# Optimization experiments

Hardware: AMD Instinct MI355X
Metric: run time of the kernel (lower is better)

The kernel has to match this reference:

```python
import jax, jax.numpy as jnp
import numpy as np

B, S, E, H = 4, 2048, 1024, 16
D = E // H
FF = 4096
LN_EPS = 1e-3  # Keras LayerNormalization default epsilon


def _layernorm(x, g, b):
    mu = jnp.mean(x, axis=-1, keepdims=True)
    var = jnp.mean(jnp.square(x - mu), axis=-1, keepdims=True)
    return (x - mu) * jax.lax.rsqrt(var + LN_EPS) * g + b


def setup_inputs() -> dict:
    key = jax.random.key(0)
    ks = jax.random.split(key, 16)
    s = lambda fan_in: 1.0 / np.sqrt(fan_in)
    inp = {
        "x": jax.random.normal(ks[0], (B, S, E), jnp.float32),
        "mask": jnp.ones((B, S), dtype=bool),
        "Wq": jax.random.normal(ks[1], (E, E), jnp.float32) * s(E),
        "bq": jnp.zeros((E,), jnp.float32),
        "Wk": jax.random.normal(ks[2], (E, E), jnp.float32) * s(E),
        "bk": jnp.zeros((E,), jnp.float32),
        "Wv": jax.random.normal(ks[3], (E, E), jnp.float32) * s(E),
        "bv": jnp.zeros((E,), jnp.float32),
        "Wo": jax.random.normal(ks[4], (E, E), jnp.float32) * s(E),
        "bo": jnp.zeros((E,), jnp.float32),
        "W1": jax.random.normal(ks[5], (E, FF), jnp.float32) * s(E),
        "b1": jnp.zeros((FF,), jnp.float32),
        "W2": jax.random.normal(ks[6], (FF, E), jnp.float32) * s(FF),
        "b2": jnp.zeros((E,), jnp.float32),
        "ln1_g": jnp.ones((E,), jnp.float32),
        "ln1_b": jnp.zeros((E,), jnp.float32),
        "ln2_g": jnp.ones((E,), jnp.float32),
        "ln2_b": jnp.zeros((E,), jnp.float32),
    }
    return inp


def reference(x, mask, Wq, bq, Wk, bk, Wv, bv, Wo, bo, W1, b1, W2, b2,
              ln1_g, ln1_b, ln2_g, ln2_b):
    # --- multi-head self attention (manual matmul + softmax + matmul) ---
    def heads(t):  # [B,S,E] -> [B,H,S,D]
        return t.reshape(B, S, H, D).transpose(0, 2, 1, 3)

    q = heads(x @ Wq + bq)
    k = heads(x @ Wk + bk)
    v = heads(x @ Wv + bv)

    scores = jnp.einsum("bhqd,bhkd->bhqk", q, k) / jnp.sqrt(jnp.float32(D))
    m = mask.astype(jnp.float32)[:, None, None, :]  # [B,1,1,S]
    scores = scores + (-1e9) * (1.0 - m)
    weights = jax.nn.softmax(scores, axis=-1)
    attn = jnp.einsum("bhqk,bhkd->bhqd", weights, v)
    attn = attn.transpose(0, 2, 1, 3).reshape(B, S, E)
    attn = attn @ Wo + bo

    # residual + layernorm (dropout is identity: training=False)
    h = _layernorm(x + attn, ln1_g, ln1_b)

    # --- FFN ---
    ff = jax.nn.relu(h @ W1 + b1) @ W2 + b2
    out = _layernorm(h + ff, ln2_g, ln2_b)
    return out
```

## Files before the change

### kernel.cpp

```cpp
#include <hip/hip_runtime.h>
#include <stdint.h>
#include <stddef.h>

#define Bn 4
#define Sn 2048
#define En 1024
#define Hn 16
#define Dn 64
#define FFn 4096
#define Mn (Bn*Sn)

typedef __bf16 bf16_t;
typedef __bf16 bf16x8 __attribute__((ext_vector_type(8)));
typedef __bf16 bf16x4 __attribute__((ext_vector_type(4)));
typedef float  f32x4  __attribute__((ext_vector_type(4)));
typedef float  f32x16 __attribute__((ext_vector_type(16)));

#define AS1 __attribute__((address_space(1)))
#define AS3 __attribute__((address_space(3)))

#define EXP2F(x) __builtin_amdgcn_exp2f(x)

static __device__ __forceinline__ void gload_lds16(const bf16_t* g, void* l) {
    __builtin_amdgcn_global_load_lds((const AS1 void*)g, (AS3 void*)l, 16, 0, 0);
}

__global__ __launch_bounds__(256)
void cvt_bf16(const float* __restrict__ xin, bf16_t* __restrict__ xout, int n)
{
    int i = (blockIdx.x * 256 + threadIdx.x) * 4;
    if (i >= n) return;
    float4 f = *(const float4*)(xin + i);
    bf16x4 o;
    o[0] = (bf16_t)f.x; o[1] = (bf16_t)f.y; o[2] = (bf16_t)f.z; o[3] = (bf16_t)f.w;
    *(bf16x4*)(xout + i) = o;
}

__global__ __launch_bounds__(256)
void transp_bf16(const float* __restrict__ W, bf16_t* __restrict__ WT, int R, int C)
{
    __shared__ float t[32][33];
    const int tx = threadIdx.x & 31, ty = threadIdx.x >> 5;
    const int c0 = blockIdx.x * 32, r0 = blockIdx.y * 32;
    #pragma unroll
    for (int i = ty; i < 32; i += 8)
        t[i][tx] = W[(size_t)(r0 + i) * C + c0 + tx];
    __syncthreads();
    #pragma unroll
    for (int i = ty; i < 32; i += 8)
        WT[(size_t)(c0 + i) * R + r0 + tx] = (bf16_t)t[tx][i];
}

__global__ __launch_bounds__(256)
void concat_bias(const float* __restrict__ a, const float* __restrict__ b,
                 const float* __restrict__ c, float* __restrict__ o)
{
    int i = blockIdx.x * 256 + threadIdx.x;
    o[i] = (i < 1024) ? a[i] : ((i < 2048) ? b[i - 1024] : c[i - 2048]);
}

template<int MODE>
__global__ __launch_bounds__(512)
void gemm3r(const bf16_t* __restrict__ A, const bf16_t* __restrict__ BT,
            const float* __restrict__ bias,
            float* __restrict__ Cf, bf16_t* __restrict__ Cb,
            int Ndim, int Kdim)
{
    extern __shared__ char smem[];
    bf16_t* lA = (bf16_t*)smem;
    bf16_t* lB = (bf16_t*)(smem + 3 * 256 * 64 * 2);

    const int tid = threadIdx.x, lane = tid & 63;
    const int w = tid >> 6, wm = w >> 1, wn = w & 1;
    const int bm = blockIdx.y, bn = blockIdx.x;

    const int srow = tid >> 3;
    const int ssl  = tid & 7;
    const int swz  = (ssl ^ (srow & 7)) * 8;
    const bf16_t* Ab = A  + (size_t)(bm * 256 + srow) * Kdim + swz;
    const bf16_t* Bb = BT + (size_t)(bn * 128 + srow) * Kdim + swz;
    const int ldst = srow * 64 + ssl * 8;

    const int ntiles = Kdim >> 6;

    f32x4 acc[4][4] = {};

    const int arow0 = (wm * 64 + (lane & 15)) * 64;
    const int brow0 = (wn * 64 + (lane & 15)) * 64;
    const int g0 = (((lane >> 4)    ) ^ (lane & 7)) * 8;
    const int g1 = ((4 + (lane >> 4)) ^ (lane & 7)) * 8;

    #define STAGE3(r, kt) do {                                                  \
        bf16_t* a_ = lA + (r) * (256 * 64) + ldst;                              \
        bf16_t* b_ = lB + (r) * (128 * 64) + ldst;                              \
        const bf16_t* ga_ = Ab + (kt) * 64;                                     \
        const bf16_t* gb_ = Bb + (kt) * 64;                                     \
        gload_lds16(ga_,                          a_);                          \
        gload_lds16(ga_ + (size_t)64  * Kdim,     a_ + 64 * 64);                \
        gload_lds16(ga_ + (size_t)128 * Kdim,     a_ + 128 * 64);               \
        gload_lds16(ga_ + (size_t)192 * Kdim,     a_ + 192 * 64);               \
        gload_lds16(gb_,                          b_);                          \
        gload_lds16(gb_ + (size_t)64  * Kdim,     b_ + 64 * 64);                \
    } while (0)

    STAGE3(0, 0);
    STAGE3(1, 1);

    for (int t = 0; t < ntiles; ++t) {
        if (t + 2 < ntiles) asm volatile("s_waitcnt vmcnt(6)" ::: "memory");
        else                asm volatile("s_waitcnt vmcnt(0)" ::: "memory");
        __builtin_amdgcn_s_barrier();
        __builtin_amdgcn_sched_barrier(0);
        if (t + 2 < ntiles) STAGE3((t + 2) % 3, t + 2);

        const bf16_t* pa = lA + (t % 3) * (256 * 64) + arow0;
        const bf16_t* pb = lB + (t % 3) * (128 * 64) + brow0;
        bf16x8 aF[4][2], bF[4][2];
        #pragma unroll
        for (int m = 0; m < 4; ++m) {
            aF[m][0] = *(const bf16x8*)(pa + m * 16 * 64 + g0);
            aF[m][1] = *(const bf16x8*)(pa + m * 16 * 64 + g1);
        }
        #pragma unroll
        for (int n = 0; n < 4; ++n) {
            bF[n][0] = *(const bf16x8*)(pb + n * 16 * 64 + g0);
            bF[n][1] = *(const bf16x8*)(pb + n * 16 * 64 + g1);
        }
        __builtin_amdgcn_s_setprio(1);
        #pragma unroll
        for (int m = 0; m < 4; ++m)
            #pragma unroll
            for (int n = 0; n < 4; ++n) {
                acc[m][n] = __builtin_amdgcn_mfma_f32_16x16x32_bf16(
                                aF[m][0], bF[n][0], acc[m][n], 0, 0, 0);
                acc[m][n] = __builtin_amdgcn_mfma_f32_16x16x32_bf16(
                                aF[m][1], bF[n][1], acc[m][n], 0, 0, 0);
            }
        __builtin_amdgcn_s_setprio(0);
    }
    #undef STAGE3

    const size_t ME = (size_t)Mn * En;
    const int fc = lane & 15;
    const int fr = (lane >> 4) * 4;
    #pragma unroll
    for (int n = 0; n < 4; ++n) {
        const int gcol = bn * 128 + wn * 64 + n * 16 + fc;
        const float bv = bias[gcol];
        #pragma unroll
        for (int m = 0; m < 4; ++m) {
            const int growb = bm * 256 + wm * 64 + m * 16 + fr;
            #pragma unroll
            for (int j = 0; j < 4; ++j) {
                const int grow = growb + j;
                float v = acc[m][n][j] + bv;
                if constexpr (MODE == 0) {
                    Cf[(size_t)grow * Ndim + gcol] = v;
                } else if constexpr (MODE == 2) {
                    Cb[(size_t)grow * Ndim + gcol] = (bf16_t)fmaxf(v, 0.f);
                } else {
                    const int id = gcol >> 10;
                    const int c1 = gcol & 1023;
                    const int b = grow >> 11, s = grow & 2047;
                    const int h = c1 >> 6,    d = c1 & 63;
                    if (id < 2)
                        Cb[(size_t)id * ME + (((size_t)(b * 16 + h) << 11) + s) * 64 + d] = (bf16_t)v;
                    else
                        Cb[2 * ME + (((size_t)(b * 16 + h) * 64 + d) << 11) + s] = (bf16_t)v;
                }
            }
        }
    }
}

static __device__ __forceinline__ uint32_t pack2_bf16(float a, float b) {
    union { bf16_t h[2]; uint32_t u; } v;
    v.h[0] = (bf16_t)a; v.h[1] = (bf16_t)b;
    return v.u;
}

#define PSWAP(a,b) asm volatile("v_permlane32_swap_b32 %0, %1" : "+v"(a), "+v"(b))

__global__ __launch_bounds__(256)
void attn_kernel(const bf16_t* __restrict__ qh, const bf16_t* __restrict__ kh,
                 const bf16_t* __restrict__ vt, bf16_t* __restrict__ attnF)
{
    __shared__ bf16_t lk[2][64 * 64];
    __shared__ bf16_t lv[2][64 * 64];

    const int tid = threadIdx.x, lane = tid & 63, w = tid >> 6;
    const int hi = lane >> 5, q = lane & 31;

    const int fid = blockIdx.x;
    const int xcd = fid & 7, idx = fid >> 3;
    const int bh  = xcd + 8 * (idx & 7);
    const int qb  = idx >> 3;
    const int q0  = qb * 128 + w * 32;

    const bf16_t* Kbase = kh + (size_t)bh * Sn * 64;
    const bf16_t* Vbase = vt + (size_t)bh * 64 * Sn;

    const float qsc = 0.125f * 1.4426950408889634f;
    bf16x8 qf[4];
    {
        const bf16_t* Qp = qh + ((size_t)bh * Sn + q0 + q) * 64 + hi * 8;
        #pragma unroll
        for (int kc = 0; kc < 4; ++kc) {
            bf16x8 r = *(const bf16x8*)(Qp + kc * 16);
            #pragma unroll
            for (int j = 0; j < 8; ++j) qf[kc][j] = (bf16_t)(qsc * (float)r[j]);
        }
    }

    const int sr = lane >> 3, ssl = lane & 7;
    const int gsoff = ((ssl ^ sr) * 8);

    f32x16 o0 = {}, o1 = {};
    float m_run = -1e30f, l_run = 0.f;

    #pragma unroll
    for (int c = 0; c < 2; ++c) {
        const int g = 2 * w + c, row = g * 8 + sr;
        gload_lds16(Kbase + (size_t)row * 64 + gsoff, &lk[0][g * 8 * 64]);
        gload_lds16(Vbase + (size_t)row * Sn + gsoff, &lv[0][g * 8 * 64]);
    }
    __syncthreads();

    int cur = 0;
    for (int it = 0; it < Sn / 64; ++it) {
        if (it + 1 < Sn / 64) {
            const int nkb = (it + 1) * 64;
            #pragma unroll
            for (int c = 0; c < 2; ++c) {
                const int g = 2 * w + c, row = g * 8 + sr;
                gload_lds16(Kbase + (size_t)(nkb + row) * 64 + gsoff, &lk[cur ^ 1][g * 8 * 64]);
                gload_lds16(Vbase + (size_t)row * Sn + nkb + gsoff,   &lv[cur ^ 1][g * 8 * 64]);
            }
        }

        f32x16 sc0 = {}, sc1 = {};
        __builtin_amdgcn_s_setprio(1);
        #pragma unroll
        for (int kc = 0; kc < 4; ++kc) {
            const int sl = ((2 * kc + hi) ^ (q & 7)) * 8;
            bf16x8 k0 = *(const bf16x8*)(&lk[cur][q * 64 + sl]);
            bf16x8 k1 = *(const bf16x8*)(&lk[cur][(32 + q) * 64 + sl]);
            sc0 = __builtin_amdgcn_mfma_f32_32x32x16_bf16(k0, qf[kc], sc0, 0, 0, 0);
            sc1 = __builtin_amdgcn_mfma_f32_32x32x16_bf16(k1, qf[kc], sc1, 0, 0, 0);
        }
        __builtin_amdgcn_s_setprio(0);

        float mx = -1e30f;
        #pragma unroll
        for (int r = 0; r < 16; ++r) mx = fmaxf(mx, fmaxf(sc0[r], sc1[r]));
        mx = fmaxf(mx, __shfl_xor(mx, 32));
        const float mnew = fmaxf(m_run, mx);
        const float corr = EXP2F(m_run - mnew);
        float p0[16], p1[16];
        float rs = 0.f;
        #pragma unroll
        for (int r = 0; r < 16; ++r) {
            p0[r] = EXP2F(sc0[r] - mnew);
            p1[r] = EXP2F(sc1[r] - mnew);
            rs += p0[r] + p1[r];
        }
        rs += __shfl_xor(rs, 32);
        l_run = l_run * corr + rs;
        m_run = mnew;
        #pragma unroll
        for (int r = 0; r < 16; ++r) { o0[r] *= corr; o1[r] *= corr; }

        bf16x8 pb[4];
        {
            union { uint32_t u[4]; bf16x8 v; } fr;
            #pragma unroll
            for (int f = 0; f < 2; ++f) {
                uint32_t u0 = pack2_bf16(p0[8*f+0], p0[8*f+1]);
                uint32_t u1 = pack2_bf16(p0[8*f+2], p0[8*f+3]);
                uint32_t u2 = pack2_bf16(p0[8*f+4], p0[8*f+5]);
                uint32_t u3 = pack2_bf16(p0[8*f+6], p0[8*f+7]);
                PSWAP(u0, u2); PSWAP(u1, u3);
                fr.u[0] = u0; fr.u[1] = u1; fr.u[2] = u2; fr.u[3] = u3;
                pb[f] = fr.v;
            }
            #pragma unroll
            for (int f = 0; f < 2; ++f) {
                uint32_t u0 = pack2_bf16(p1[8*f+0], p1[8*f+1]);
                uint32_t u1 = pack2_bf16(p1[8*f+2], p1[8*f+3]);
                uint32_t u2 = pack2_bf16(p1[8*f+4], p1[8*f+5]);
                uint32_t u3 = pack2_bf16(p1[8*f+6], p1[8*f+7]);
                PSWAP(u0, u2); PSWAP(u1, u3);
                fr.u[0] = u0; fr.u[1] = u1; fr.u[2] = u2; fr.u[3] = u3;
                pb[2 + f] = fr.v;
            }
        }

        __builtin_amdgcn_s_setprio(1);
        #pragma unroll
        for (int sk = 0; sk < 4; ++sk) {
            const int sl = ((2 * sk + hi) ^ (q & 7)) * 8;
            bf16x8 v0 = *(const bf16x8*)(&lv[cur][q * 64 + sl]);
            bf16x8 v1 = *(const bf16x8*)(&lv[cur][(32 + q) * 64 + sl]);
            o0 = __builtin_amdgcn_mfma_f32_32x32x16_bf16(v0, pb[sk], o0, 0, 0, 0);
            o1 = __builtin_amdgcn_mfma_f32_32x32x16_bf16(v1, pb[sk], o1, 0, 0, 0);
        }
        __builtin_amdgcn_s_setprio(0);

        __syncthreads();
        cur ^= 1;
    }

    const float linv = 1.f / l_run;
    const int b = bh >> 4, h = bh & 15;
    bf16_t* dst = attnF + ((size_t)b * Sn + q0 + q) * En + h * 64;
    #pragma unroll
    for (int grp = 0; grp < 4; ++grp) {
        bf16x4 w0, w1;
        #pragma unroll
        for (int j = 0; j < 4; ++j) {
            w0[j] = (bf16_t)(o0[4 * grp + j] * linv);
            w1[j] = (bf16_t)(o1[4 * grp + j] * linv);
        }
        *(bf16x4*)(dst + grp * 8 + 4 * hi)      = w0;
        *(bf16x4*)(dst + 32 + grp * 8 + 4 * hi) = w1;
    }
}

__global__ __launch_bounds__(256)
void ln_kernel(const float* __restrict__ res, const float* __restrict__ proj,
               const float* __restrict__ gamma, const float* __restrict__ beta,
               float* __restrict__ outf, bf16_t* __restrict__ outb)
{
    const int row = blockIdx.x;
    const int tid = threadIdx.x;
    const size_t base = (size_t)row * En + tid * 4;
    float v[4];
    #pragma unroll
    for (int i = 0; i < 4; ++i)
        v[i] = res[base + i] + proj[base + i];

    float s = 0.f, ss = 0.f;
    #pragma unroll
    for (int i = 0; i < 4; ++i) { s += v[i]; ss += v[i] * v[i]; }
    #pragma unroll
    for (int off = 1; off < 64; off <<= 1) {
        s  += __shfl_xor(s, off);
        ss += __shfl_xor(ss, off);
    }
    __shared__ float sm[8];
    const int wv = tid >> 6;
    if ((tid & 63) == 0) { sm[wv] = s; sm[4 + wv] = ss; }
    __syncthreads();
    s  = sm[0] + sm[1] + sm[2] + sm[3];
    ss = sm[4] + sm[5] + sm[6] + sm[7];
    const float mu   = s * (1.f / En);
    const float var  = ss * (1.f / En) - mu * mu;
    const float rstd = rsqrtf(var + 1e-3f);
    #pragma unroll
    for (int i = 0; i < 4; ++i) {
        const int c = tid * 4 + i;
        const float o = (v[i] - mu) * rstd * gamma[c] + beta[c];
        if (outf) outf[base + i] = o;
        if (outb) outb[base + i] = (bf16_t)o;
    }
}

extern "C" void kernel_launch(void* const* d_in, const int* in_sizes, int n_in,
                              void* d_out, int out_size, void* d_ws, size_t ws_size,
                              hipStream_t stream)
{
    (void)in_sizes; (void)n_in; (void)out_size; (void)ws_size;
    const float* x   = (const float*)d_in[0];
    const float* Wq  = (const float*)d_in[2];
    const float* bq  = (const float*)d_in[3];
    const float* Wk  = (const float*)d_in[4];
    const float* bk  = (const float*)d_in[5];
    const float* Wv  = (const float*)d_in[6];
    const float* bv  = (const float*)d_in[7];
    const float* Wo  = (const float*)d_in[8];
    const float* bo  = (const float*)d_in[9];
    const float* W1  = (const float*)d_in[10];
    const float* b1  = (const float*)d_in[11];
    const float* W2  = (const float*)d_in[12];
    const float* b2  = (const float*)d_in[13];
    const float* g1  = (const float*)d_in[14];
    const float* be1 = (const float*)d_in[15];
    const float* g2  = (const float*)d_in[16];
    const float* be2 = (const float*)d_in[17];
    float* out = (float*)d_out;

    char* p = (char*)d_ws;
    const size_t ME = (size_t)Mn * En;
    bf16_t* xb    = (bf16_t*)p;  p += ME * 2;
    bf16_t* WqT   = (bf16_t*)p;  p += (size_t)En * En * 2;
    bf16_t* WkT   = (bf16_t*)p;  p += (size_t)En * En * 2;
    bf16_t* WvT   = (bf16_t*)p;  p += (size_t)En * En * 2;
    bf16_t* WoT   = (bf16_t*)p;  p += (size_t)En * En * 2;
    bf16_t* W1T   = (bf16_t*)p;  p += (size_t)FFn * En * 2;
    bf16_t* W2T   = (bf16_t*)p;  p += (size_t)En * FFn * 2;
    bf16_t* qh    = (bf16_t*)p;  p += ME * 2;
    bf16_t* kh    = (bf16_t*)p;  p += ME * 2;
    bf16_t* vt    = (bf16_t*)p;  p += ME * 2;
    bf16_t* attnF = (bf16_t*)p;  p += ME * 2;
    bf16_t* hb    = (bf16_t*)p;  p += ME * 2;
    bf16_t* ff    = (bf16_t*)p;  p += (size_t)Mn * FFn * 2;
    float*  bqkv  = (float*)p;   p += 3072 * 4;
    float*  hf32  = (float*)qh;

    const dim3 blk(256);
    const int GEMM_LDS = (3 * 256 * 64 + 3 * 128 * 64) * 2;

    static bool attr_done = false;
    if (!attr_done) {
        hipFuncSetAttribute((const void*)gemm3r<0>, hipFuncAttributeMaxDynamicSharedMemorySize, GEMM_LDS);
        hipFuncSetAttribute((const void*)gemm3r<2>, hipFuncAttributeMaxDynamicSharedMemorySize, GEMM_LDS);
        hipFuncSetAttribute((const void*)gemm3r<5>, hipFuncAttributeMaxDynamicSharedMemorySize, GEMM_LDS);
        attr_done = true;
    }

    cvt_bf16<<<dim3(Mn * En / 1024), blk, 0, stream>>>(x, xb, Mn * En);
    transp_bf16<<<dim3(32, 32),  blk, 0, stream>>>(Wq, WqT, En, En);
    transp_bf16<<<dim3(32, 32),  blk, 0, stream>>>(Wk, WkT, En, En);
    transp_bf16<<<dim3(32, 32),  blk, 0, stream>>>(Wv, WvT, En, En);
    transp_bf16<<<dim3(32, 32),  blk, 0, stream>>>(Wo, WoT, En, En);
    transp_bf16<<<dim3(128, 32), blk, 0, stream>>>(W1, W1T, En, FFn);
    transp_bf16<<<dim3(32, 128), blk, 0, stream>>>(W2, W2T, FFn, En);
    concat_bias<<<dim3(12), blk, 0, stream>>>(bq, bk, bv, bqkv);

    gemm3r<5><<<dim3(24, 32), dim3(512), GEMM_LDS, stream>>>(xb, WqT, bqkv, nullptr, qh, 3072, En);

    attn_kernel<<<dim3(1024), blk, 0, stream>>>(qh, kh, vt, attnF);

    gemm3r<0><<<dim3(8, 32), dim3(512), GEMM_LDS, stream>>>(attnF, WoT, bo, out, nullptr, En, En);
    ln_kernel<<<dim3(Mn), blk, 0, stream>>>(x, out, g1, be1, hf32, hb);

    gemm3r<2><<<dim3(32, 32), dim3(512), GEMM_LDS, stream>>>(hb, W1T, b1, nullptr, ff, FFn, En);
    gemm3r<0><<<dim3(8, 32), dim3(512), GEMM_LDS, stream>>>(ff, W2T, b2, out, nullptr, En, FFn);

    ln_kernel<<<dim3(Mn), blk, 0, stream>>>(hf32, out, g2, be2, out, nullptr);
}
```

Before: 510.6 us.

## Split GEMM k-tile into two halves interleaving prefetch, add lazy softmax rescale

The GEMM main loop now splits each 64-wide k-tile into two halves, issuing half of the next tile's global-to-LDS loads before each half's MFMAs, with extra barriers between them. The aim is to spread memory traffic across the compute and lower register pressure from fragments. The attention kernel skips the running-max update and output rescale when the new block max exceeds the current one by at most 8 (log2 units), which saves exp and multiply work but adds a branch and a wave vote. The extra barriers per tile may add synchronisation cost.

```diff
diff --git a/kernel.cpp b/kernel.cpp
--- a/kernel.cpp
+++ b/kernel.cpp
@@ -90,11 +90,11 @@
     const int g0 = (((lane >> 4)    ) ^ (lane & 7)) * 8;
     const int g1 = ((4 + (lane >> 4)) ^ (lane & 7)) * 8;
 
-    #define STAGE3(r, kt) do {                                                  \
+    #define STAGE_ALL(r, kt) do {                                              \
         bf16_t* a_ = lA + (r) * (256 * 64) + ldst;                              \
         bf16_t* b_ = lB + (r) * (128 * 64) + ldst;                              \
-        const bf16_t* ga_ = Ab + (kt) * 64;                                     \
-        const bf16_t* gb_ = Bb + (kt) * 64;                                     \
+        const bf16_t* ga_ = Ab + (size_t)(kt) * 64;                             \
+        const bf16_t* gb_ = Bb + (size_t)(kt) * 64;                             \
         gload_lds16(ga_,                          a_);                          \
         gload_lds16(ga_ + (size_t)64  * Kdim,     a_ + 64 * 64);                \
         gload_lds16(ga_ + (size_t)128 * Kdim,     a_ + 128 * 64);               \
@@ -103,42 +103,76 @@
         gload_lds16(gb_ + (size_t)64  * Kdim,     b_ + 64 * 64);                \
     } while (0)
 
-    STAGE3(0, 0);
-    STAGE3(1, 1);
+    STAGE_ALL(0, 0);
+    STAGE_ALL(1, 1);
 
     for (int t = 0; t < ntiles; ++t) {
         if (t + 2 < ntiles) asm volatile("s_waitcnt vmcnt(6)" ::: "memory");
         else                asm volatile("s_waitcnt vmcnt(0)" ::: "memory");
         __builtin_amdgcn_s_barrier();
         __builtin_amdgcn_sched_barrier(0);
-        if (t + 2 < ntiles) STAGE3((t + 2) % 3, t + 2);
 
         const bf16_t* pa = lA + (t % 3) * (256 * 64) + arow0;
         const bf16_t* pb = lB + (t % 3) * (128 * 64) + brow0;
-        bf16x8 aF[4][2], bF[4][2];
-        #pragma unroll
-        for (int m = 0; m < 4; ++m) {
-            aF[m][0] = *(const bf16x8*)(pa + m * 16 * 64 + g0);
-            aF[m][1] = *(const bf16x8*)(pa + m * 16 * 64 + g1);
-        }
-        #pragma unroll
-        for (int n = 0; n < 4; ++n) {
-            bF[n][0] = *(const bf16x8*)(pb + n * 16 * 64 + g0);
-            bF[n][1] = *(const bf16x8*)(pb + n * 16 * 64 + g1);
-        }
-        __builtin_amdgcn_s_setprio(1);
-        #pragma unroll
-        for (int m = 0; m < 4; ++m)
-            #pragma unroll
-            for (int n = 0; n < 4; ++n) {
-                acc[m][n] = __builtin_amdgcn_mfma_f32_16x16x32_bf16(
-                                aF[m][0], bF[n][0], acc[m][n], 0, 0, 0);
-                acc[m][n] = __builtin_amdgcn_mfma_f32_16x16x32_bf16(
-                                aF[m][1], bF[n][1], acc[m][n], 0, 0, 0);
-            }
-        __builtin_amdgcn_s_setprio(0);
-    }
-    #undef STAGE3
+        const bool pf = (t + 2) < ntiles;
+        const bf16_t* ga = Ab + (size_t)(t + 2) * 64;
+        const bf16_t* gb = Bb + (size_t)(t + 2) * 64;
+        bf16_t* sa = lA + ((t + 2) % 3) * (256 * 64) + ldst;
+        bf16_t* sb = lB + ((t + 2) % 3) * (128 * 64) + ldst;
+
+        {
+            bf16x8 aF[4], bF[4];
+            #pragma unroll
+            for (int m = 0; m < 4; ++m)
+                aF[m] = *(const bf16x8*)(pa + m * 16 * 64 + g0);
+            #pragma unroll
+            for (int n = 0; n < 4; ++n)
+                bF[n] = *(const bf16x8*)(pb + n * 16 * 64 + g0);
+            if (pf) {
+                gload_lds16(ga,                      sa);
+                gload_lds16(ga + (size_t)64 * Kdim,  sa + 64 * 64);
+                gload_lds16(gb,                      sb);
+            }
+            __builtin_amdgcn_s_barrier();
+            __builtin_amdgcn_sched_barrier(0);
+            __builtin_amdgcn_s_setprio(1);
+            #pragma unroll
+            for (int m = 0; m < 4; ++m)
+                #pragma unroll
+                for (int n = 0; n < 4; ++n)
+                    acc[m][n] = __builtin_amdgcn_mfma_f32_16x16x32_bf16(
+                                    aF[m], bF[n], acc[m][n], 0, 0, 0);
+            __builtin_amdgcn_s_setprio(0);
+            __builtin_amdgcn_s_barrier();
+            __builtin_amdgcn_sched_barrier(0);
+        }
+
+        {
+            bf16x8 aF[4], bF[4];
+            #pragma unroll
+            for (int m = 0; m < 4; ++m)
+                aF[m] = *(const bf16x8*)(pa + m * 16 * 64 + g1);
+            #pragma unroll
+            for (int n = 0; n < 4; ++n)
+                bF[n] = *(const bf16x8*)(pb + n * 16 * 64 + g1);
+            if (pf) {
+                gload_lds16(ga + (size_t)128 * Kdim, sa + 128 * 64);
+                gload_lds16(ga + (size_t)192 * Kdim, sa + 192 * 64);
+                gload_lds16(gb + (size_t)64 * Kdim,  sb + 64 * 64);
+            }
+            __builtin_amdgcn_s_barrier();
+            __builtin_amdgcn_sched_barrier(0);
+            __builtin_amdgcn_s_setprio(1);
+            #pragma unroll
+            for (int m = 0; m < 4; ++m)
+                #pragma unroll
+                for (int n = 0; n < 4; ++n)
+                    acc[m][n] = __builtin_amdgcn_mfma_f32_16x16x32_bf16(
+                                    aF[m], bF[n], acc[m][n], 0, 0, 0);
+            __builtin_amdgcn_s_setprio(0);
+        }
+    }
+    #undef STAGE_ALL
 
     const size_t ME = (size_t)Mn * En;
     const int fc = lane & 15;
@@ -254,21 +288,33 @@
         #pragma unroll
         for (int r = 0; r < 16; ++r) mx = fmaxf(mx, fmaxf(sc0[r], sc1[r]));
         mx = fmaxf(mx, __shfl_xor(mx, 32));
-        const float mnew = fmaxf(m_run, mx);
-        const float corr = EXP2F(m_run - mnew);
+
         float p0[16], p1[16];
         float rs = 0.f;
-        #pragma unroll
-        for (int r = 0; r < 16; ++r) {
-            p0[r] = EXP2F(sc0[r] - mnew);
-            p1[r] = EXP2F(sc1[r] - mnew);
-            rs += p0[r] + p1[r];
-        }
-        rs += __shfl_xor(rs, 32);
-        l_run = l_run * corr + rs;
-        m_run = mnew;
-        #pragma unroll
-        for (int r = 0; r < 16; ++r) { o0[r] *= corr; o1[r] *= corr; }
+        if (__all(mx - m_run <= 8.0f)) {
+            #pragma unroll
+            for (int r = 0; r < 16; ++r) {
+                p0[r] = EXP2F(sc0[r] - m_run);
+                p1[r] = EXP2F(sc1[r] - m_run);
+                rs += p0[r] + p1[r];
+            }
+            rs += __shfl_xor(rs, 32);
+            l_run += rs;
+        } else {
+            const float mnew = fmaxf(m_run, mx);
+            const float corr = EXP2F(m_run - mnew);
+            #pragma unroll
+            for (int r = 0; r < 16; ++r) {
+                p0[r] = EXP2F(sc0[r] - mnew);
+                p1[r] = EXP2F(sc1[r] - mnew);
+                rs += p0[r] + p1[r];
+            }
+            rs += __shfl_xor(rs, 32);
+            l_run = l_run * corr + rs;
+            m_run = mnew;
+            #pragma unroll
+            for (int r = 0; r < 16; ++r) { o0[r] *= corr; o1[r] *= corr; }
+        }
 
         bf16x8 pb[4];
         {
```

New measurement: 520.4 us. No clear change (+1.9%).
